# Optimization experiments

Hardware: AMD Instinct MI355X
Metric: run time of the kernel (lower is better)

## Reference

```python
import jax, jax.numpy as jnp
import numpy as np

B, K, E, D = 256, 2, 16, 512  # batch, top_k, num_experts, input_dim==output_dim
EPS = 1e-5  # nn.LayerNorm default eps
SCALE = 0.02  # param init scale


def setup_inputs() -> dict:
    key = jax.random.key(0)
    ks = jax.random.split(key, 9)
    return {
        "x": jax.random.normal(ks[0], (B, D), dtype=jnp.float32),
        "weight_probs": jax.random.uniform(ks[1], (B, K), dtype=jnp.float32),
        "bias_probs": jax.random.uniform(ks[2], (B, K), dtype=jnp.float32),
        "input_weight_bank": jax.random.normal(ks[3], (E, D, D), dtype=jnp.float32) * SCALE,
        "output_weight_bank": jax.random.normal(ks[4], (E, D, D), dtype=jnp.float32) * SCALE,
        "diagonal_weight_bank": jax.random.normal(ks[5], (E, D, D), dtype=jnp.float32) * SCALE,
        "bias_bank": jax.random.normal(ks[6], (E, D, D), dtype=jnp.float32) * SCALE,
        "weight_indices": jax.random.randint(ks[7], (B, K), 0, E),
        "bias_indices": jax.random.randint(ks[8], (B, K), 0, E),
    }


def reference(x, weight_probs, bias_probs, input_weight_bank, output_weight_bank,
              diagonal_weight_bank, bias_bank, weight_indices, bias_indices):
    # gather per-example expert parameter slabs: [B, K, D, D]
    iv = jnp.einsum('bi,bkij->bkj', x, input_weight_bank[weight_indices])     # [B,K,D]
    ov = jnp.einsum('bi,bkij->bkj', x, output_weight_bank[weight_indices])    # [B,K,D]
    dv = jnp.einsum('bi,bkij->bkj', x, diagonal_weight_bank[weight_indices])  # [B,K,D]

    # outer-product generated weight matrix + dynamic diagonal (in==out, no padding)
    outer = iv[..., :, None] * ov[..., None, :]                               # [B,K,D,D]
    r = jnp.arange(D)
    W = outer.at[..., r, r].add(dv)                                           # add diag embed

    # probability-weighted combine over top-k (weight_probs reshaped (-1,K,1,1) in torch)
    Wmix = jnp.einsum('bk,bkio->bio', weight_probs, W)                        # [B,D,D]

    # LayerNorm over output_dim, elementwise_affine=False
    mu = jnp.mean(Wmix, axis=-1, keepdims=True)
    var = jnp.var(Wmix, axis=-1, keepdims=True)
    Wn = (Wmix - mu) * jax.lax.rsqrt(var + EPS)

    # generated biases: gather + einsum + weighted combine ((-1,K,1) reshape)
    bv = jnp.einsum('bi,bkio->bko', x, bias_bank[bias_indices])               # [B,K,D]
    bmix = jnp.einsum('bk,bko->bo', bias_probs, bv)                           # [B,D]
    return (Wn, bmix)
```

## Files before the change

### kernel.cpp

```cpp
#include <hip/hip_runtime.h>
#include <math.h>

#define BB 256
#define KK 2
#define EE 16
#define DD 512
#define BK (BB*KK)

#define WCH 18432
#define BCH 18560
#define WS_F_BASE 20480
#define SLAB (BK*DD)

__global__ void build_lists(const int* __restrict__ widx,
                            const int* __restrict__ bidx,
                            int* __restrict__ ws) {
    __shared__ int scw[16], scb[16];
    int* wlist = ws + 1024;
    int* blist = ws + 10240;
    const int t = threadIdx.x;
    if (t < 16) { scw[t] = 0; scb[t] = 0; }
    __syncthreads();
    int e = widx[t];
    int p = atomicAdd(&scw[e], 1);
    wlist[e * BK + p] = t;
    int eb = bidx[t];
    int pb = atomicAdd(&scb[eb], 1);
    blist[eb * BK + pb] = t;
    __syncthreads();
    if (t == 0) {
        int nc = 0;
        for (int e2 = 0; e2 < 16; ++e2) {
            int n = scw[e2];
            for (int r = 0; r < n; r += 16)
                ws[WCH + 1 + nc++] = e2 | (r << 8) | (min(16, n - r) << 20);
        }
        ws[WCH] = nc;
    }
    if (t == 64) {
        int nc = 0;
        for (int e2 = 0; e2 < 16; ++e2) {
            int n = scb[e2];
            for (int r = 0; r < n; r += 16)
                ws[BCH + 1 + nc++] = e2 | (r << 8) | (min(16, n - r) << 20);
        }
        ws[BCH] = nc;
    }
}

__launch_bounds__(256)
__global__ void expert_vm(const float* __restrict__ x,
                          const float* __restrict__ w_in,
                          const float* __restrict__ w_out,
                          const float* __restrict__ w_diag,
                          const float* __restrict__ w_bias,
                          const int* __restrict__ ws_i,
                          float* __restrict__ ws_f) {
    const int z = blockIdx.z;
    const int* ch = ws_i + ((z < 3) ? WCH : BCH);
    const int slot = blockIdx.y;
    if (slot >= ch[0]) return;
    const int desc = ch[1 + slot];
    const int e = desc & 0xff, r0 = (desc >> 8) & 0xfff, rows = desc >> 20;
    const int* list = ws_i + ((z < 3) ? 1024 : 10240) + e * BK + r0;
    const float* W = (z == 0 ? w_in : z == 1 ? w_out : z == 2 ? w_diag : w_bias)
                     + (size_t)e * DD * DD;
    float* out = ws_f + WS_F_BASE + (size_t)z * SLAB;

    __shared__ int plist[16];
    __shared__ float4 xs[DD][4];
    const int t = threadIdx.x;
    if (t < 16) plist[t] = (t < rows) ? list[t] : -1;
    __syncthreads();
    #pragma unroll
    for (int k = 0; k < 8; ++k) {
        int idx = t + k * 256;
        int i = idx >> 2, q = idx & 3;
        int p0 = plist[q * 4 + 0], p1 = plist[q * 4 + 1];
        int p2 = plist[q * 4 + 2], p3 = plist[q * 4 + 3];
        float4 v;
        v.x = (p0 >= 0) ? x[(p0 >> 1) * DD + i] : 0.f;
        v.y = (p1 >= 0) ? x[(p1 >> 1) * DD + i] : 0.f;
        v.z = (p2 >= 0) ? x[(p2 >> 1) * DD + i] : 0.f;
        v.w = (p3 >= 0) ? x[(p3 >> 1) * DD + i] : 0.f;
        xs[i][q] = v;
    }
    __syncthreads();

    const int col = blockIdx.x * 128 + (t & 127);
    const int h = t >> 7;
    const float* Wc = W + col;
    float a0 = 0, a1 = 0, a2 = 0, a3 = 0, b0 = 0, b1 = 0, b2 = 0, b3 = 0;
    #pragma unroll 8
    for (int i = 0; i < DD; ++i) {
        float w = Wc[(size_t)i * DD];
        float4 xa = xs[i][2 * h];
        float4 xb = xs[i][2 * h + 1];
        a0 += xa.x * w; a1 += xa.y * w; a2 += xa.z * w; a3 += xa.w * w;
        b0 += xb.x * w; b1 += xb.y * w; b2 += xb.z * w; b3 += xb.w * w;
    }
    float accs[8] = {a0, a1, a2, a3, b0, b1, b2, b3};
    #pragma unroll
    for (int r = 0; r < 8; ++r) {
        int p = plist[h * 8 + r];
        if (p >= 0) out[(size_t)p * DD + col] = accs[r];
    }
}

__launch_bounds__(256)
__global__ void gen_write(const float* __restrict__ ws_f,
                          const float* __restrict__ wp,
                          float* __restrict__ outp) {
    const int b = blockIdx.y;
    const int chunk = blockIdx.x;
    const float* iv  = ws_f + WS_F_BASE;
    const float* ovs = iv + SLAB;
    const float* dvs = ovs + SLAB;

    __shared__ float4 ov1v[128], ov2v[128];
    __shared__ float S[5], red[20];
    __shared__ float sa1[64], sa2[64], sdd[64], smu[64], srs[64];
    const int t = threadIdx.x;
    const float* ov1 = (const float*)ov1v;
    const float* ov2 = (const float*)ov2v;

    const float4* ovp0 = (const float4*)(ovs + (size_t)(b * 2 + 0) * DD);
    const float4* ovp1 = (const float4*)(ovs + (size_t)(b * 2 + 1) * DD);
    if (t < 128) ov1v[t] = ovp0[t];
    else         ov2v[t - 128] = ovp1[t - 128];
    __syncthreads();

    float v0a = ov1[t], v0b = ov1[t + 256], v1a = ov2[t], v1b = ov2[t + 256];
    float s[5];
    s[0] = v0a + v0b;
    s[1] = v1a + v1b;
    s[2] = v0a * v0a + v0b * v0b;
    s[3] = v0a * v1a + v0b * v1b;
    s[4] = v1a * v1a + v1b * v1b;
    #pragma unroll
    for (int off = 32; off; off >>= 1) {
        #pragma unroll
        for (int q = 0; q < 5; ++q) s[q] += __shfl_down(s[q], off);
    }
    const int lane = t & 63, wv = t >> 6;
    if (lane == 0) {
        #pragma unroll
        for (int q = 0; q < 5; ++q) red[wv * 5 + q] = s[q];
    }
    __syncthreads();
    if (t == 0) {
        #pragma unroll
        for (int q = 0; q < 5; ++q) S[q] = red[q] + red[5 + q] + red[10 + q] + red[15 + q];
    }
    __syncthreads();

    if (t < 64) {
        const float S1 = S[0], S2 = S[1], S11 = S[2], S12 = S[3], S22 = S[4];
        int i = chunk * 64 + t;
        float wp0 = wp[b * 2], wp1 = wp[b * 2 + 1];
        float a1 = wp0 * iv[(size_t)(b * 2 + 0) * DD + i];
        float a2 = wp1 * iv[(size_t)(b * 2 + 1) * DD + i];
        float dd = wp0 * dvs[(size_t)(b * 2 + 0) * DD + i]
                 + wp1 * dvs[(size_t)(b * 2 + 1) * DD + i];
        float mu = (a1 * S1 + a2 * S2 + dd) * (1.0f / DD);
        float e2 = (a1 * a1 * S11 + 2.0f * a1 * a2 * S12 + a2 * a2 * S22
                    + 2.0f * (a1 * ov1[i] + a2 * ov2[i]) * dd + dd * dd) * (1.0f / DD);
        float var = e2 - mu * mu;
        sa1[t] = a1; sa2[t] = a2; sdd[t] = dd; smu[t] = mu;
        srs[t] = rsqrtf(var + 1e-5f);
    }
    __syncthreads();

    const int ci = t & 127, rh = t >> 7;
    const float4 o1 = ov1v[ci], o2 = ov2v[ci];
    const int jj = ci * 4;
    float* obase = outp + ((size_t)b * DD + chunk * 64) * DD;
    #pragma unroll 2
    for (int rr = 0; rr < 32; ++rr) {
        int r = rr * 2 + rh;
        int irow = chunk * 64 + r;
        float a1 = sa1[r], a2 = sa2[r], dd = sdd[r], mu = smu[r], rs = srs[r];
        float4 w;
        w.x = a1 * o1.x + a2 * o2.x + ((irow == jj)     ? dd : 0.f);
        w.y = a1 * o1.y + a2 * o2.y + ((irow == jj + 1) ? dd : 0.f);
        w.z = a1 * o1.z + a2 * o2.z + ((irow == jj + 2) ? dd : 0.f);
        w.w = a1 * o1.w + a2 * o2.w + ((irow == jj + 3) ? dd : 0.f);
        w.x = (w.x - mu) * rs; w.y = (w.y - mu) * rs;
        w.z = (w.z - mu) * rs; w.w = (w.w - mu) * rs;
        ((float4*)(obase + (size_t)r * DD))[ci] = w;
    }
}

__global__ void bias_mix(const float* __restrict__ ws_f,
                         const float* __restrict__ bp,
                         float* __restrict__ outp) {
    const float* bv = ws_f + WS_F_BASE + 3 * (size_t)SLAB;
    int b = blockIdx.x;
    int t = threadIdx.x;
    float p0 = bp[b * 2], p1 = bp[b * 2 + 1];
    const float* b0 = bv + (size_t)(b * 2 + 0) * DD;
    const float* b1 = bv + (size_t)(b * 2 + 1) * DD;
    outp[(size_t)b * DD + t]       = p0 * b0[t]       + p1 * b1[t];
    outp[(size_t)b * DD + t + 256] = p0 * b0[t + 256] + p1 * b1[t + 256];
}

extern "C" void kernel_launch(void* const* d_in, const int* in_sizes, int n_in,
                              void* d_out, int out_size, void* d_ws, size_t ws_size,
                              hipStream_t stream) {
    const float* x      = (const float*)d_in[0];
    const float* wprobs = (const float*)d_in[1];
    const float* bprobs = (const float*)d_in[2];
    const float* w_in   = (const float*)d_in[3];
    const float* w_out  = (const float*)d_in[4];
    const float* w_diag = (const float*)d_in[5];
    const float* w_bias = (const float*)d_in[6];
    const int*   widx   = (const int*)d_in[7];
    const int*   bidx   = (const int*)d_in[8];
    float* out = (float*)d_out;
    int*   wsI = (int*)d_ws;
    float* wsF = (float*)d_ws;

    build_lists<<<1, BK, 0, stream>>>(widx, bidx, wsI);

    expert_vm<<<dim3(4, 48, 4), 256, 0, stream>>>(x, w_in, w_out, w_diag, w_bias,
                                                  wsI, wsF);

    gen_write<<<dim3(8, BB), 256, 0, stream>>>(wsF, wprobs, out);

    bias_mix<<<BB, 256, 0, stream>>>(wsF, bprobs, out + (size_t)BB * DD * DD);
}
```

Measured before the change: 414.5 us.

## Split expert GEMV reduction dimension into four partial slabs summed downstream

The expert_vm kernel now splits the 512-long input dimension into four 128-row partitions, launching four times as many blocks. Each block writes a partial result to its own workspace slab. The consumer kernels (gen_write, bias_mix) sum the four partials when they read. This targets low occupancy and the long serial loop in the GEMV. In exchange it adds workspace traffic and extra reads in the downstream kernels.

```diff
diff --git a/kernel.cpp b/kernel.cpp
--- a/kernel.cpp
+++ b/kernel.cpp
@@ -6,6 +6,7 @@
 #define EE 16
 #define DD 512
 #define BK (BB*KK)
+#define NP 4
 
 #define WCH 18432
 #define BCH 18560
@@ -56,33 +57,35 @@
                           const float* __restrict__ w_bias,
                           const int* __restrict__ ws_i,
                           float* __restrict__ ws_f) {
-    const int z = blockIdx.z;
+    const int zp = blockIdx.z;
+    const int z = zp >> 2, ip = zp & 3;
     const int* ch = ws_i + ((z < 3) ? WCH : BCH);
     const int slot = blockIdx.y;
     if (slot >= ch[0]) return;
     const int desc = ch[1 + slot];
     const int e = desc & 0xff, r0 = (desc >> 8) & 0xfff, rows = desc >> 20;
     const int* list = ws_i + ((z < 3) ? 1024 : 10240) + e * BK + r0;
+    const int i0 = ip * 128;
     const float* W = (z == 0 ? w_in : z == 1 ? w_out : z == 2 ? w_diag : w_bias)
-                     + (size_t)e * DD * DD;
-    float* out = ws_f + WS_F_BASE + (size_t)z * SLAB;
+                     + (size_t)e * DD * DD + (size_t)i0 * DD;
+    float* out = ws_f + WS_F_BASE + (size_t)zp * SLAB;
 
     __shared__ int plist[16];
-    __shared__ float4 xs[DD][4];
+    __shared__ float4 xs[128][4];
     const int t = threadIdx.x;
     if (t < 16) plist[t] = (t < rows) ? list[t] : -1;
     __syncthreads();
     #pragma unroll
-    for (int k = 0; k < 8; ++k) {
+    for (int k = 0; k < 2; ++k) {
         int idx = t + k * 256;
         int i = idx >> 2, q = idx & 3;
         int p0 = plist[q * 4 + 0], p1 = plist[q * 4 + 1];
         int p2 = plist[q * 4 + 2], p3 = plist[q * 4 + 3];
         float4 v;
-        v.x = (p0 >= 0) ? x[(p0 >> 1) * DD + i] : 0.f;
-        v.y = (p1 >= 0) ? x[(p1 >> 1) * DD + i] : 0.f;
-        v.z = (p2 >= 0) ? x[(p2 >> 1) * DD + i] : 0.f;
-        v.w = (p3 >= 0) ? x[(p3 >> 1) * DD + i] : 0.f;
+        v.x = (p0 >= 0) ? x[(p0 >> 1) * DD + i0 + i] : 0.f;
+        v.y = (p1 >= 0) ? x[(p1 >> 1) * DD + i0 + i] : 0.f;
+        v.z = (p2 >= 0) ? x[(p2 >> 1) * DD + i0 + i] : 0.f;
+        v.w = (p3 >= 0) ? x[(p3 >> 1) * DD + i0 + i] : 0.f;
         xs[i][q] = v;
     }
     __syncthreads();
@@ -91,8 +94,8 @@
     const int h = t >> 7;
     const float* Wc = W + col;
     float a0 = 0, a1 = 0, a2 = 0, a3 = 0, b0 = 0, b1 = 0, b2 = 0, b3 = 0;
-    #pragma unroll 8
-    for (int i = 0; i < DD; ++i) {
+    #pragma unroll 16
+    for (int i = 0; i < 128; ++i) {
         float w = Wc[(size_t)i * DD];
         float4 xa = xs[i][2 * h];
         float4 xb = xs[i][2 * h + 1];
@@ -113,9 +116,7 @@
                           float* __restrict__ outp) {
     const int b = blockIdx.y;
     const int chunk = blockIdx.x;
-    const float* iv  = ws_f + WS_F_BASE;
-    const float* ovs = iv + SLAB;
-    const float* dvs = ovs + SLAB;
+    const float* base = ws_f + WS_F_BASE;
 
     __shared__ float4 ov1v[128], ov2v[128];
     __shared__ float S[5], red[20];
@@ -124,10 +125,20 @@
     const float* ov1 = (const float*)ov1v;
     const float* ov2 = (const float*)ov2v;
 
-    const float4* ovp0 = (const float4*)(ovs + (size_t)(b * 2 + 0) * DD);
-    const float4* ovp1 = (const float4*)(ovs + (size_t)(b * 2 + 1) * DD);
-    if (t < 128) ov1v[t] = ovp0[t];
-    else         ov2v[t - 128] = ovp1[t - 128];
+    {
+        const int tt = t & 127;
+        const int row = b * 2 + (t >> 7);
+        float sx = 0.f, sy = 0.f, sz = 0.f, sw = 0.f;
+        #pragma unroll
+        for (int pp = 0; pp < NP; ++pp) {
+            const float4* q4 = (const float4*)(base + (size_t)(4 + pp) * SLAB
+                                               + (size_t)row * DD);
+            float4 v = q4[tt];
+            sx += v.x; sy += v.y; sz += v.z; sw += v.w;
+        }
+        float4 s = make_float4(sx, sy, sz, sw);
+        if (t < 128) ov1v[tt] = s; else ov2v[tt] = s;
+    }
     __syncthreads();
 
     float v0a = ov1[t], v0b = ov1[t + 256], v1a = ov2[t], v1b = ov2[t + 256];
@@ -158,10 +169,19 @@
         const float S1 = S[0], S2 = S[1], S11 = S[2], S12 = S[3], S22 = S[4];
         int i = chunk * 64 + t;
         float wp0 = wp[b * 2], wp1 = wp[b * 2 + 1];
-        float a1 = wp0 * iv[(size_t)(b * 2 + 0) * DD + i];
-        float a2 = wp1 * iv[(size_t)(b * 2 + 1) * DD + i];
-        float dd = wp0 * dvs[(size_t)(b * 2 + 0) * DD + i]
-                 + wp1 * dvs[(size_t)(b * 2 + 1) * DD + i];
+        float iv1 = 0.f, iv2 = 0.f, dv1 = 0.f, dv2 = 0.f;
+        #pragma unroll
+        for (int pp = 0; pp < NP; ++pp) {
+            const float* s0 = base + (size_t)(0 + pp) * SLAB;
+            const float* s2 = base + (size_t)(8 + pp) * SLAB;
+            iv1 += s0[(size_t)(b * 2 + 0) * DD + i];
+            iv2 += s0[(size_t)(b * 2 + 1) * DD + i];
+            dv1 += s2[(size_t)(b * 2 + 0) * DD + i];
+            dv2 += s2[(size_t)(b * 2 + 1) * DD + i];
+        }
+        float a1 = wp0 * iv1;
+        float a2 = wp1 * iv2;
+        float dd = wp0 * dv1 + wp1 * dv2;
         float mu = (a1 * S1 + a2 * S2 + dd) * (1.0f / DD);
         float e2 = (a1 * a1 * S11 + 2.0f * a1 * a2 * S12 + a2 * a2 * S22
                     + 2.0f * (a1 * ov1[i] + a2 * ov2[i]) * dd + dd * dd) * (1.0f / DD);
@@ -194,14 +214,21 @@
 __global__ void bias_mix(const float* __restrict__ ws_f,
                          const float* __restrict__ bp,
                          float* __restrict__ outp) {
-    const float* bv = ws_f + WS_F_BASE + 3 * (size_t)SLAB;
+    const float* base = ws_f + WS_F_BASE;
     int b = blockIdx.x;
     int t = threadIdx.x;
     float p0 = bp[b * 2], p1 = bp[b * 2 + 1];
-    const float* b0 = bv + (size_t)(b * 2 + 0) * DD;
-    const float* b1 = bv + (size_t)(b * 2 + 1) * DD;
-    outp[(size_t)b * DD + t]       = p0 * b0[t]       + p1 * b1[t];
-    outp[(size_t)b * DD + t + 256] = p0 * b0[t + 256] + p1 * b1[t + 256];
+    float s0a = 0.f, s0b = 0.f, s1a = 0.f, s1b = 0.f;
+    #pragma unroll
+    for (int pp = 0; pp < NP; ++pp) {
+        const float* bv = base + (size_t)(12 + pp) * SLAB;
+        s0a += bv[(size_t)(b * 2 + 0) * DD + t];
+        s0b += bv[(size_t)(b * 2 + 0) * DD + t + 256];
+        s1a += bv[(size_t)(b * 2 + 1) * DD + t];
+        s1b += bv[(size_t)(b * 2 + 1) * DD + t + 256];
+    }
+    outp[(size_t)b * DD + t]       = p0 * s0a + p1 * s1a;
+    outp[(size_t)b * DD + t + 256] = p0 * s0b + p1 * s1b;
 }
 
 extern "C" void kernel_launch(void* const* d_in, const int* in_sizes, int n_in,
@@ -222,8 +249,8 @@
 
     build_lists<<<1, BK, 0, stream>>>(widx, bidx, wsI);
 
-    expert_vm<<<dim3(4, 48, 4), 256, 0, stream>>>(x, w_in, w_out, w_diag, w_bias,
-                                                  wsI, wsF);
+    expert_vm<<<dim3(4, 48, 16), 256, 0, stream>>>(x, w_in, w_out, w_diag, w_bias,
+                                                   wsI, wsF);
 
     gen_write<<<dim3(8, BB), 256, 0, stream>>>(wsF, wprobs, out);
 
```

New measurement: 396.5 us. 1.05x faster.
